# Kernel tuning notes

Hardware: AMD Instinct MI355X
Metric: run time of the kernel (lower is better)

## Reference

```python
import jax, jax.numpy as jnp
import numpy as np

DIM = 128
K = 4
B, H, W = 2, 256, 256
DEFORM_WEIGHT = 0.3


def conv2d(x, w, b, pad):
    # x [B,C,H,W], w [O,I,kh,kw], stride 1
    y = jax.lax.conv_general_dilated(
        x, w, (1, 1), [(pad, pad), (pad, pad)],
        dimension_numbers=('NCHW', 'OIHW', 'NCHW'))
    return y + b[None, :, None, None]


def gelu(x):
    return jax.nn.gelu(x, approximate=False)  # torch nn.GELU default (erf)


def grid_sample_k(feat, grid):
    """Bilinear grid_sample, padding_mode='border', align_corners=True.
    feat: [B,C,H,W]; grid: [B,K,H,W,2] (x,y) in [-1,1]. Returns [B,C,K,H,W]."""
    Bn, C, Hh, Ww = feat.shape
    px = (grid[..., 0] + 1.0) * 0.5 * (Ww - 1)
    py = (grid[..., 1] + 1.0) * 0.5 * (Hh - 1)
    px = jnp.clip(px, 0.0, Ww - 1)
    py = jnp.clip(py, 0.0, Hh - 1)
    x0 = jnp.floor(px).astype(jnp.int32)
    y0 = jnp.floor(py).astype(jnp.int32)
    x1 = jnp.minimum(x0 + 1, Ww - 1)
    y1 = jnp.minimum(y0 + 1, Hh - 1)
    wx = (px - x0)[:, None]  # [B,1,K,H,W]
    wy = (py - y0)[:, None]
    featf = feat.reshape(Bn, C, Hh * Ww)

    def gather(yi, xi):
        idx = (yi * Ww + xi).reshape(Bn, -1)  # [B, K*H*W]
        g = jax.vmap(lambda f, i: f[:, i])(featf, idx)  # [B,C,K*H*W]
        return g.reshape(Bn, C, *yi.shape[1:])

    v00 = gather(y0, x0)
    v01 = gather(y0, x1)
    v10 = gather(y1, x0)
    v11 = gather(y1, x1)
    return (v00 * (1 - wx) * (1 - wy) + v01 * wx * (1 - wy)
            + v10 * (1 - wx) * wy + v11 * wx * wy)


def setup_inputs() -> dict:
    key = jax.random.key(0)
    ks = jax.random.split(key, 16)
    nrm = lambda k, shape, s: jax.random.normal(k, shape, dtype=jnp.float32) * s
    return {
        'query_feat': jax.random.normal(ks[0], (B, DIM, H, W), dtype=jnp.float32),
        'key_feat': jax.random.normal(ks[1], (B, DIM, H, W), dtype=jnp.float32),
        # offset_net: Conv(dim,dim,3) -> GELU -> Conv(dim,2K,3); small scale keeps offsets sane
        'ow1': nrm(ks[2], (DIM, DIM, 3, 3), 0.02), 'ob1': jnp.zeros((DIM,), jnp.float32),
        'ow2': nrm(ks[3], (2 * K, DIM, 3, 3), 0.01), 'ob2': jnp.zeros((2 * K,), jnp.float32),
        # weight_net: Conv(dim,dim//4,3) -> GELU -> Conv(dim//4,K,1)
        'ww1': nrm(ks[4], (DIM // 4, DIM, 3, 3), 0.05), 'wb1': jnp.zeros((DIM // 4,), jnp.float32),
        'ww2': nrm(ks[5], (K, DIM // 4, 1, 1), 0.05), 'wb2': jnp.zeros((K,), jnp.float32),
        # fusion_conv: Conv(dim,dim,1) -> GELU -> Conv(dim,dim,1)
        'fw1': nrm(ks[6], (DIM, DIM, 1, 1), 0.05), 'fb1': jnp.zeros((DIM,), jnp.float32),
        'fw2': nrm(ks[7], (DIM, DIM, 1, 1), 0.05), 'fb2': jnp.zeros((DIM,), jnp.float32),
    }


def reference(query_feat, key_feat, ow1, ob1, ow2, ob2, ww1, wb1, ww2, wb2,
              fw1, fb1, fw2, fb2):
    offsets = conv2d(gelu(conv2d(query_feat, ow1, ob1, 1)), ow2, ob2, 1)  # [B,2K,H,W]
    wlog = conv2d(gelu(conv2d(query_feat, ww1, wb1, 1)), ww2, wb2, 0)     # [B,K,H,W]
    Bn, C, Hh, Ww = key_feat.shape
    Kp = wlog.shape[1]
    off = offsets.reshape(Bn, Kp, 2, Hh, Ww).transpose(0, 1, 3, 4, 2)  # [B,K,H,W,2]
    gy, gx = jnp.meshgrid(jnp.linspace(-1.0, 1.0, Hh),
                          jnp.linspace(-1.0, 1.0, Ww), indexing='ij')
    base = jnp.stack([gx, gy], axis=-1).astype(off.dtype)  # [H,W,2] (x,y)
    scale = jnp.array([Ww / 2.0, Hh / 2.0], dtype=off.dtype)
    grid = jnp.clip(base + off / scale, -1.0, 1.0)  # [B,K,H,W,2]
    sampled = grid_sample_k(key_feat, grid)  # [B,C,K,H,W]
    wsoft = jax.nn.softmax(wlog, axis=1)[:, None]  # [B,1,K,H,W]
    agg = (sampled * wsoft).sum(axis=2)  # [B,C,H,W]
    fused = conv2d(gelu(conv2d(agg, fw1, fb1, 0)), fw2, fb2, 0)
    return query_feat + fused * DEFORM_WEIGHT
```

## Files before the change

kernel.cpp:

```cpp
#include <hip/hip_runtime.h>
#include <hip/hip_fp16.h>

typedef unsigned short u16;
typedef __attribute__((ext_vector_type(8))) short bf16x8;
typedef __attribute__((ext_vector_type(4))) float f32x4;

constexpr int B_ = 2, C_ = 128, H_ = 256, W_ = 256, P_ = H_ * W_;
constexpr int HP_ = 258, WP_ = 258;

union HU { __half2 h; unsigned int u; };

__device__ __forceinline__ float bf2f(u16 u) {
  union { unsigned int i; float f; } v; v.i = ((unsigned int)u) << 16; return v.f;
}
__device__ __forceinline__ u16 f2bf(float f) {
  union { float f; unsigned int i; } v; v.f = f;
  return (u16)((v.i + 0x7fffu + ((v.i >> 16) & 1u)) >> 16);
}
__device__ __forceinline__ float gelu_f(float x) {
  float u = x * (1.5957691216057308f + 0.071354816272f * x * x);
  return x / (1.0f + __expf(-u));
}

__device__ __forceinline__ void async16(const u16* g, u16* l) {
  __builtin_amdgcn_global_load_lds(
      (const __attribute__((address_space(1))) unsigned int*)g,
      (__attribute__((address_space(3))) unsigned int*)l, 16, 0, 0);
}

__global__ __launch_bounds__(256) void prologue(
    const float* __restrict__ q, const float* __restrict__ key,
    const float* __restrict__ ow1, const float* __restrict__ ow2,
    const float* __restrict__ ww1, const float* __restrict__ fw1,
    const float* __restrict__ fw2,
    u16* __restrict__ qpad, u16* __restrict__ keyn, u16* __restrict__ t1pad,
    u16* __restrict__ wb) {
  __shared__ u16 l[64 * 66];
  const int id = blockIdx.x, tid = threadIdx.x;
  if (id < 8192) {
    int z = id >> 10, r = id & 1023;
    int bx = r & 3, by = r >> 2;
    const float* in; u16* out; int OW, opad;
    if (z < 4) { in = q; out = qpad; OW = WP_; opad = 1; }
    else { z -= 4; in = key; out = keyn; OW = W_; opad = 0; }
    int b = z >> 1, c0 = (z & 1) * 64;
    int h = by, w0 = bx * 64;
    for (int it = 0; it < 4; ++it) {
      int lin = it * 256 + tid;
      int c = lin >> 4, w4 = (lin & 15) * 4;
      float4 v = *(const float4*)&in[(((size_t)b * C_ + c0 + c) * H_ + h) * W_ + w0 + w4];
      l[c * 66 + w4 + 0] = f2bf(v.x);
      l[c * 66 + w4 + 1] = f2bf(v.y);
      l[c * 66 + w4 + 2] = f2bf(v.z);
      l[c * 66 + w4 + 3] = f2bf(v.w);
    }
    __syncthreads();
    int OH = (opad ? HP_ : H_);
    for (int it = 0; it < 8; ++it) {
      int lin = it * 256 + tid;
      int w = lin >> 5, c = (lin & 31) * 2;
      unsigned val = (unsigned)l[c * 66 + w] | ((unsigned)l[(c + 1) * 66 + w] << 16);
      *(unsigned*)&out[(((size_t)b * OH + h + opad) * OW + (w0 + w + opad)) * C_ + c0 + c] = val;
    }
  } else if (id < 10256) {
    int j = id - 8192;
    u16* buf = (j < 1032) ? qpad : t1pad;
    int idx = ((j < 1032) ? j : j - 1032) * 256 + tid;
    int c = idx & 127;
    int t = idx >> 7;
    int pos = t % 258;
    int side = (t / 258) & 3;
    int b = t / (258 * 4);
    int h, w;
    if (side == 0) { h = 0; w = pos; }
    else if (side == 1) { h = 257; w = pos; }
    else if (side == 2) { h = pos; w = 0; }
    else { h = pos; w = 257; }
    buf[(((size_t)b * HP_ + h) * WP_ + w) * C_ + c] = 0;
  } else {
    int idx = (id - 10256) * 256 + tid;
    float v;
    if (idx < 184320) {
      int e = idx & 7, lr = (idx >> 3) & 15, kb = (idx >> 7) & 3;
      int t = idx >> 9;
      int g = t % 10, u = t / 10;
      int cq = u & 3, tap = u >> 2;
      int ci = cq * 32 + kb * 8 + e, co = g * 16 + lr;
      v = (co < 128) ? ow1[(co * 128 + ci) * 9 + tap]
                     : ww1[((co - 128) * 128 + ci) * 9 + tap];
    } else if (idx < 202752) {
      int j = idx - 184320;
      int e = j & 7, lr = (j >> 3) & 15, kb = (j >> 7) & 3;
      int cq = (j >> 9) & 3, tap = j >> 11;
      int ci = cq * 32 + kb * 8 + e, co = lr;
      v = (co < 8) ? ow2[(co * 128 + ci) * 9 + tap] : 0.0f;
    } else if (idx < 219136) {
      v = fw1[idx - 202752];
    } else {
      v = fw2[idx - 219136];
    }
    wb[idx] = f2bf(v);
  }
}

__global__ __launch_bounds__(512, 4) void conv3_big(
    const u16* __restrict__ A, const u16* __restrict__ Wf,
    const float* __restrict__ bias1, const float* __restrict__ bias2,
    u16* __restrict__ outb, u16* __restrict__ outw) {
  constexpr int RPX = 36, ROWU = RPX * 32;
  __shared__ __align__(16) u16 As[6 * ROWU];
  const int tid = threadIdx.x, lane = tid & 63, wave = tid >> 6;
  const int id = blockIdx.x;
  const int s = id >> 3;
  const int h0 = (((id & 7) << 3) | (s & 7)) << 2;
  const int w0 = ((s >> 3) & 7) << 5;
  const int b = s >> 6;
  const int wr = wave >> 1, wc = wave & 1;
  const int wn = wc * 80;
  const int lr = lane & 15, kq = lane >> 4;
  const int gbase = wn >> 4;

  int preA[2][3];
#pragma unroll
  for (int i = 0; i < 2; i++)
#pragma unroll
    for (int kx = 0; kx < 3; kx++) {
      int pxv = i * 16 + lr + kx;
      preA[i][kx] = (pxv * 4 + (kq ^ ((pxv >> 1) & 3))) * 8;
    }

  f32x4 acc[2][5];
#pragma unroll
  for (int i = 0; i < 2; i++)
#pragma unroll
    for (int j = 0; j < 5; j++) { f32x4 z = {0.f, 0.f, 0.f, 0.f}; acc[i][j] = z; }

  for (int cq = 0; cq < 4; ++cq) {
    const int ci0 = cq * 32;
    __syncthreads();
    for (int i = tid; i < 864; i += 512) {
      int ry = i / 144;
      int rem = i - ry * 144;
      int px = rem >> 2, c8 = rem & 3;
      int g = c8 ^ ((px >> 1) & 3);
      async16(A + ((size_t)(b * HP_ + h0 + ry) * WP_ + (w0 + px)) * 128 + ci0 + g * 8,
              As + i * 8);
    }
    __syncthreads();
#pragma unroll
    for (int tap = 0; tap < 9; ++tap) {
      const int ky = tap / 3, kx = tap % 3;
      bf16x8 bfr[5], af[2];
#pragma unroll
      for (int j = 0; j < 5; ++j)
        bfr[j] = *(const bf16x8*)&Wf[(size_t)((((tap * 4 + cq) * 10 + gbase + j) * 4 + kq) * 16 + lr) * 8];
#pragma unroll
      for (int i = 0; i < 2; ++i)
        af[i] = *(const bf16x8*)&As[(wr + ky) * ROWU + preA[i][kx]];
#pragma unroll
      for (int i = 0; i < 2; i++)
#pragma unroll
        for (int j = 0; j < 5; j++)
          acc[i][j] = __builtin_amdgcn_mfma_f32_16x16x32_bf16(af[i], bfr[j], acc[i][j], 0, 0, 0);
    }
  }

  const int h = h0 + wr;
#pragma unroll
  for (int i = 0; i < 2; i++) {
#pragma unroll
    for (int j = 0; j < 5; j++) {
      const int co = wn + j * 16 + lr;
#pragma unroll
      for (int r = 0; r < 4; r++) {
        const int w = w0 + i * 16 + kq * 4 + r;
        float v = acc[i][j][r];
        if (co < 128) {
          v = gelu_f(v + bias1[co]);
          outb[(((size_t)b * HP_ + h + 1) * WP_ + (w + 1)) * 128 + co] = f2bf(v);
        } else {
          v = gelu_f(v + bias2[co - 128]);
          outw[((size_t)b * P_ + (size_t)h * W_ + w) * 32 + (co - 128)] = f2bf(v);
        }
      }
    }
  }
}

__global__ __launch_bounds__(256) void conv_off(
    const u16* __restrict__ A, const u16* __restrict__ Wf,
    const float* __restrict__ bias,
    const u16* __restrict__ w1b, const float* __restrict__ ww2,
    const float* __restrict__ wb2, uint4* __restrict__ desc) {
  constexpr int RPX = 66, ROWU = RPX * 32;
  __shared__ __align__(16) u16 As[2][6 * ROWU];
  float* off_lds = (float*)As;
  const int tid = threadIdx.x, lane = tid & 63, wave = tid >> 6;
  const int id = blockIdx.x;
  const int s = id >> 3;
  const int h0 = (((id & 7) << 3) | (s & 7)) << 2;
  const int w0 = ((s >> 3) & 3) << 6;
  const int b = s >> 5;
  const int lr = lane & 15, kq = lane >> 4;

  int preA[4][3];
#pragma unroll
  for (int i = 0; i < 4; i++)
#pragma unroll
    for (int kx = 0; kx < 3; kx++) {
      int pxv = i * 16 + lr + kx;
      preA[i][kx] = (pxv * 4 + (kq ^ ((pxv >> 1) & 3))) * 8;
    }

  f32x4 acc[4];
#pragma unroll
  for (int i = 0; i < 4; i++) { f32x4 z = {0.f, 0.f, 0.f, 0.f}; acc[i] = z; }

  for (int r = 0; r < 2; ++r) {
    __syncthreads();
#pragma unroll
    for (int half = 0; half < 2; ++half) {
      const int ci0 = (r * 2 + half) * 32;
      for (int i = tid; i < 1584; i += 256) {
        int ry = i / 264;
        int rem = i - ry * 264;
        int px = rem >> 2, c8 = rem & 3;
        int g = c8 ^ ((px >> 1) & 3);
        async16(A + ((size_t)(b * HP_ + h0 + ry) * WP_ + (w0 + px)) * 128 + ci0 + g * 8,
                As[half] + i * 8);
      }
    }
    __syncthreads();
#pragma unroll
    for (int half = 0; half < 2; ++half) {
      const int cq = r * 2 + half;
      const u16* Ac = As[half];
#pragma unroll
      for (int tap = 0; tap < 9; ++tap) {
        const int ky = tap / 3, kx = tap % 3;
        bf16x8 bw = *(const bf16x8*)&Wf[(size_t)(((tap * 4 + cq) * 4 + kq) * 16 + lr) * 8];
        bf16x8 af[4];
#pragma unroll
        for (int i = 0; i < 4; ++i)
          af[i] = *(const bf16x8*)&Ac[(wave + ky) * ROWU + preA[i][kx]];
#pragma unroll
        for (int i = 0; i < 4; i++)
          acc[i] = __builtin_amdgcn_mfma_f32_16x16x32_bf16(af[i], bw, acc[i], 0, 0, 0);
      }
    }
  }

  __syncthreads();
#pragma unroll
  for (int i = 0; i < 4; i++) {
#pragma unroll
    for (int r = 0; r < 4; r++) {
      if (lr < 8) {
        int px = i * 16 + (lane >> 4) * 4 + r;
        off_lds[(wave * 64 + px) * 9 + lr] = acc[i][r] + bias[lr];
      }
    }
  }
  __syncthreads();

  const int pp = tid;
  const int h = h0 + (pp >> 6), w = w0 + (pp & 63);
  const int pix = b * P_ + h * W_ + w;
  const u16* wp = w1b + (size_t)pix * 32;
  float f[32];
#pragma unroll
  for (int i = 0; i < 32; i += 2) {
    unsigned u = *(const unsigned*)&wp[i];
    f[i] = bf2f((u16)u); f[i + 1] = bf2f((u16)(u >> 16));
  }
  float lg[4];
#pragma unroll
  for (int k = 0; k < 4; k++) {
    float sacc = wb2[k];
#pragma unroll
    for (int i = 0; i < 32; i++) sacc = fmaf(ww2[k * 32 + i], f[i], sacc);
    lg[k] = sacc;
  }
  float mx = fmaxf(fmaxf(lg[0], lg[1]), fmaxf(lg[2], lg[3]));
  float e[4], sum = 0.f;
#pragma unroll
  for (int k = 0; k < 4; k++) { e[k] = __expf(lg[k] - mx); sum += e[k]; }
  const float inv = 1.0f / sum;
#pragma unroll
  for (int k = 0; k < 4; k++) {
    float ox = off_lds[pp * 9 + 2 * k], oy = off_lds[pp * 9 + 2 * k + 1];
    float gx = (2.0f * w / 255.0f - 1.0f) + ox * (1.0f / 128.0f);
    float gy = (2.0f * h / 255.0f - 1.0f) + oy * (1.0f / 128.0f);
    gx = fminf(fmaxf(gx, -1.f), 1.f);
    gy = fminf(fmaxf(gy, -1.f), 1.f);
    float px = fminf(fmaxf((gx + 1.f) * 127.5f, 0.f), 255.f);
    float py = fminf(fmaxf((gy + 1.f) * 127.5f, 0.f), 255.f);
    int x0 = (int)px, y0 = (int)py;
    int x1 = min(x0 + 1, 255), y1 = min(y0 + 1, 255);
    float wx = px - x0, wy = py - y0;
    float wk = e[k] * inv;
    float w00 = (1.f - wx) * (1.f - wy) * wk, w01 = wx * (1.f - wy) * wk;
    float w10 = (1.f - wx) * wy * wk,         w11 = wx * wy * wk;
    HU t01, t23;
    t01.h = __floats2half2_rn(w00, w01);
    t23.h = __floats2half2_rn(w10, w11);
    uint4 d;
    d.x = (unsigned)(y0 * 256 + x0) | ((unsigned)(x1 - x0) << 16) | ((unsigned)(y1 - y0) << 17);
    d.y = t01.u; d.z = t23.u; d.w = 0;
    desc[(size_t)pix * 4 + k] = d;
  }
}

__global__ __launch_bounds__(512, 4) void sample_fuse(
    const uint4* __restrict__ desc, const u16* __restrict__ keyn,
    const u16* __restrict__ W1, const u16* __restrict__ W2,
    const float* __restrict__ b1, const float* __restrict__ b2,
    const float* __restrict__ resid, float* __restrict__ out) {
  __shared__ __align__(16) u16 SM[128 * 128];
  __shared__ __align__(16) u16 T2[128 * 136];
  const int tid = threadIdx.x, lane = tid & 63, wave = tid >> 6;
  const int h = blockIdx.y, w0 = blockIdx.x * 128;
  const int b = blockIdx.z;
  const int wr = wave >> 1, wc = wave & 1;
  const int wm = wr * 32, wn = wc * 64;
  const int lr = lane & 15, kq = lane >> 4;
  const int sw = lr & 7;

  {
    const u16* kb = keyn + (size_t)b * (P_ * C_) + 2 * lane;
    const int pxbase = wave * 16;
    const int pixs = __builtin_amdgcn_readfirstlane(b * P_ + h * W_ + w0 + pxbase);
    const int half64 = (lane >> 5) * 64;
    const int gg = (lane >> 2) & 7;
    const int e2 = (lane & 3) * 2;
    for (int p = 0; p < 16; p += 2) {
      uint4 dA[4], dB[4];
#pragma unroll
      for (int k = 0; k < 4; ++k) dA[k] = desc[(size_t)(pixs + p) * 4 + k];
#pragma unroll
      for (int k = 0; k < 4; ++k) dB[k] = desc[(size_t)(pixs + p + 1) * 4 + k];
      unsigned vA[4][4], vB[4][4];
#pragma unroll
      for (int k = 0; k < 4; ++k) {
        const u16* c0 = kb + ((int)(dA[k].x & 0xFFFFu) << 7);
        const int o01 = (int)((dA[k].x >> 16) & 1u) << 7;
        const int o10 = (int)((dA[k].x >> 17) & 1u) << 15;
        vA[k][0] = *(const unsigned*)(c0);
        vA[k][1] = *(const unsigned*)(c0 + o01);
        vA[k][2] = *(const unsigned*)(c0 + o10);
        vA[k][3] = *(const unsigned*)(c0 + o10 + o01);
      }
#pragma unroll
      for (int k = 0; k < 4; ++k) {
        const u16* c0 = kb + ((int)(dB[k].x & 0xFFFFu) << 7);
        const int o01 = (int)((dB[k].x >> 16) & 1u) << 7;
        const int o10 = (int)((dB[k].x >> 17) & 1u) << 15;
        vB[k][0] = *(const unsigned*)(c0);
        vB[k][1] = *(const unsigned*)(c0 + o01);
        vB[k][2] = *(const unsigned*)(c0 + o10);
        vB[k][3] = *(const unsigned*)(c0 + o10 + o01);
      }
      float p0A[4], p1A[4], p0B[4], p1B[4];
#pragma unroll
      for (int k = 0; k < 4; ++k) {
        HU t01, t23; t01.u = dA[k].y; t23.u = dA[k].z;
        float2 wA = __half22float2(t01.h);
        float2 wB = __half22float2(t23.h);
        float s0 = wA.x * bf2f((u16)vA[k][0]);
        s0 = fmaf(wA.y, bf2f((u16)vA[k][1]), s0);
        s0 = fmaf(wB.x, bf2f((u16)vA[k][2]), s0);
        s0 = fmaf(wB.y, bf2f((u16)vA[k][3]), s0);
        p0A[k] = s0;
        float s1 = wA.x * bf2f((u16)(vA[k][0] >> 16));
        s1 = fmaf(wA.y, bf2f((u16)(vA[k][1] >> 16)), s1);
        s1 = fmaf(wB.x, bf2f((u16)(vA[k][2] >> 16)), s1);
        s1 = fmaf(wB.y, bf2f((u16)(vA[k][3] >> 16)), s1);
        p1A[k] = s1;
      }
#pragma unroll
      for (int k = 0; k < 4; ++k) {
        HU t01, t23; t01.u = dB[k].y; t23.u = dB[k].z;
        float2 wA = __half22float2(t01.h);
        float2 wB = __half22float2(t23.h);
        float s0 = wA.x * bf2f((u16)vB[k][0]);
        s0 = fmaf(wA.y, bf2f((u16)vB[k][1]), s0);
        s0 = fmaf(wB.x, bf2f((u16)vB[k][2]), s0);
        s0 = fmaf(wB.y, bf2f((u16)vB[k][3]), s0);
        p0B[k] = s0;
        float s1 = wA.x * bf2f((u16)(vB[k][0] >> 16));
        s1 = fmaf(wA.y, bf2f((u16)(vB[k][1] >> 16)), s1);
        s1 = fmaf(wB.x, bf2f((u16)(vB[k][2] >> 16)), s1);
        s1 = fmaf(wB.y, bf2f((u16)(vB[k][3] >> 16)), s1);
        p1B[k] = s1;
      }
      float a0A = (p0A[0] + p0A[1]) + (p0A[2] + p0A[3]);
      float a1A = (p1A[0] + p1A[1]) + (p1A[2] + p1A[3]);
      float a0B = (p0B[0] + p0B[1]) + (p0B[2] + p0B[3]);
      float a1B = (p1B[0] + p1B[1]) + (p1B[2] + p1B[3]);
      const int pxA = pxbase + p, pxB = pxbase + p + 1;
      unsigned uA = ((unsigned)f2bf(a1A) << 16) | (unsigned)f2bf(a0A);
      unsigned uB = ((unsigned)f2bf(a1B) << 16) | (unsigned)f2bf(a0B);
      *(unsigned*)&SM[pxA * 128 + half64 + ((gg ^ (pxA & 7)) << 3) + e2] = uA;
      *(unsigned*)&SM[pxB * 128 + half64 + ((gg ^ (pxB & 7)) << 3) + e2] = uB;
    }
  }

  f32x4 acc[2][4];
#pragma unroll
  for (int i = 0; i < 2; i++)
#pragma unroll
    for (int j = 0; j < 4; j++) { f32x4 z = {0.f, 0.f, 0.f, 0.f}; acc[i][j] = z; }

  for (int c = 0; c < 2; ++c) {
    const int ci0 = c << 6;
    const u16* Wb = W1 + ci0;
    __syncthreads();
    for (int i = tid; i < 1024; i += 512) {
      int r = i >> 3, cb = i & 7;
      async16(Wb + r * 128 + ((cb ^ (r & 7)) << 3), T2 + i * 8);
    }
    __syncthreads();
#pragma unroll
    for (int ks = 0; ks < 2; ++ks) {
      const int kb = ks * 4 + kq;
      bf16x8 af[2], bfr[4];
#pragma unroll
      for (int i = 0; i < 2; i++)
        af[i] = *(const bf16x8*)&SM[(wm + i * 16 + lr) * 128 + ci0 + ((kb ^ sw) << 3)];
#pragma unroll
      for (int j = 0; j < 4; j++)
        bfr[j] = *(const bf16x8*)&T2[(wn + j * 16 + lr) * 64 + ((kb ^ sw) << 3)];
#pragma unroll
      for (int i = 0; i < 2; i++)
#pragma unroll
        for (int j = 0; j < 4; j++)
          acc[i][j] = __builtin_amdgcn_mfma_f32_16x16x32_bf16(af[i], bfr[j], acc[i][j], 0, 0, 0);
    }
  }
  __syncthreads();

  for (int i = tid; i < 2048; i += 512) {
    int r = i >> 4, sl = i & 15;
    int g = sl ^ (r & 7);
    async16(W2 + r * 128 + g * 8, SM + i * 8);
  }
#pragma unroll
  for (int i = 0; i < 2; i++)
#pragma unroll
    for (int j = 0; j < 4; j++) {
      const int co = wn + j * 16 + lr;
#pragma unroll
      for (int r = 0; r < 4; r++) {
        const int px = wm + i * 16 + kq * 4 + r;
        T2[px * 136 + co] = f2bf(gelu_f(acc[i][j][r] + b1[co]));
      }
    }
  __syncthreads();

#pragma unroll
  for (int i = 0; i < 2; i++)
#pragma unroll
    for (int j = 0; j < 4; j++) { f32x4 z = {0.f, 0.f, 0.f, 0.f}; acc[i][j] = z; }
#pragma unroll
  for (int ks = 0; ks < 4; ++ks) {
    const int kc = ks * 4 + kq;
    bf16x8 af[2], bfr[4];
#pragma unroll
    for (int i = 0; i < 2; i++)
      af[i] = *(const bf16x8*)&T2[(wm + i * 16 + lr) * 136 + kc * 8];
#pragma unroll
    for (int j = 0; j < 4; j++) {
      int rr = wn + j * 16 + lr;
      bfr[j] = *(const bf16x8*)&SM[rr * 128 + (kc ^ (rr & 7)) * 8];
    }
#pragma unroll
    for (int i = 0; i < 2; i++)
#pragma unroll
      for (int j = 0; j < 4; j++)
        acc[i][j] = __builtin_amdgcn_mfma_f32_16x16x32_bf16(af[i], bfr[j], acc[i][j], 0, 0, 0);
  }

#pragma unroll
  for (int i = 0; i < 2; i++) {
#pragma unroll
    for (int j = 0; j < 4; j++) {
      const int co = wn + j * 16 + lr;
      const int w = w0 + wm + i * 16 + kq * 4;
      size_t idx = ((size_t)b * 128 + co) * (size_t)P_ + (size_t)h * W_ + w;
      float4 rv = *(const float4*)&resid[idx];
      float bi = b2[co];
      float4 ov;
      ov.x = rv.x + 0.3f * (acc[i][j][0] + bi);
      ov.y = rv.y + 0.3f * (acc[i][j][1] + bi);
      ov.z = rv.z + 0.3f * (acc[i][j][2] + bi);
      ov.w = rv.w + 0.3f * (acc[i][j][3] + bi);
      *(float4*)&out[idx] = ov;
    }
  }
}

extern "C" void kernel_launch(void* const* d_in, const int* in_sizes, int n_in,
                              void* d_out, int out_size, void* d_ws, size_t ws_size,
                              hipStream_t stream) {
  (void)in_sizes; (void)n_in; (void)out_size; (void)ws_size;
  const float* q   = (const float*)d_in[0];
  const float* key = (const float*)d_in[1];
  const float* ow1 = (const float*)d_in[2];
  const float* ob1 = (const float*)d_in[3];
  const float* ow2 = (const float*)d_in[4];
  const float* ob2 = (const float*)d_in[5];
  const float* ww1 = (const float*)d_in[6];
  const float* wb1 = (const float*)d_in[7];
  const float* ww2 = (const float*)d_in[8];
  const float* wb2 = (const float*)d_in[9];
  const float* fw1 = (const float*)d_in[10];
  const float* fb1 = (const float*)d_in[11];
  const float* fw2 = (const float*)d_in[12];
  const float* fb2 = (const float*)d_in[13];
  float* out = (float*)d_out;
  char* ws = (char*)d_ws;

  u16* qpad  = (u16*)(ws);
  u16* t1pad = (u16*)(ws + 34080768);
  u16* keyn  = (u16*)(ws + 68161536);
  u16* w1b   = (u16*)(ws + 101715968);
  u16* wbuf  = (u16*)(ws + 110104576);
  uint4* desc = (uint4*)ws;

  prologue<<<11176, 256, 0, stream>>>(q, key, ow1, ow2, ww1, fw1, fw2,
                                      qpad, keyn, t1pad, wbuf);
  conv3_big<<<1024, 512, 0, stream>>>(qpad, wbuf, ob1, wb1, t1pad, w1b);
  conv_off<<<512, 256, 0, stream>>>(t1pad, wbuf + 184320, ob2, w1b, ww2, wb2, desc);
  sample_fuse<<<dim3(2, 256, 2), 512, 0, stream>>>(desc, keyn, wbuf + 202752,
                                                   wbuf + 219136, fb1, fb2, q, out);
}
```

Baseline: 345.0 us.

## Double-buffer activations and weights in LDS with async prefetch in conv3_big

Result: no change. 340.8 us (-1.2%).

```diff
diff --git a/kernel.cpp b/kernel.cpp
--- a/kernel.cpp
+++ b/kernel.cpp
@@ -108,7 +108,9 @@
     const float* __restrict__ bias1, const float* __restrict__ bias2,
     u16* __restrict__ outb, u16* __restrict__ outw) {
   constexpr int RPX = 36, ROWU = RPX * 32;
-  __shared__ __align__(16) u16 As[6 * ROWU];
+  constexpr int WTILE = 5120;
+  __shared__ __align__(16) u16 As[2][6 * ROWU];
+  __shared__ __align__(16) u16 Wl[2][WTILE];
   const int tid = threadIdx.x, lane = tid & 63, wave = tid >> 6;
   const int id = blockIdx.x;
   const int s = id >> 3;
@@ -129,39 +131,79 @@
       preA[i][kx] = (pxv * 4 + (kq ^ ((pxv >> 1) & 3))) * 8;
     }
 
+  size_t soff0, soff1;
+  int doff0, doff1;
+  const bool has2 = (tid + 512 < 864);
+  {
+    int i = tid;
+    int ry = i / 144;
+    int rem = i - ry * 144;
+    int px = rem >> 2, c8 = rem & 3;
+    int g = c8 ^ ((px >> 1) & 3);
+    soff0 = ((size_t)(b * HP_ + h0 + ry) * WP_ + (w0 + px)) * 128 + g * 8;
+    doff0 = i * 8;
+  }
+  {
+    int i = (tid + 512 < 864) ? tid + 512 : tid;
+    int ry = i / 144;
+    int rem = i - ry * 144;
+    int px = rem >> 2, c8 = rem & 3;
+    int g = c8 ^ ((px >> 1) & 3);
+    soff1 = ((size_t)(b * HP_ + h0 + ry) * WP_ + (w0 + px)) * 128 + g * 8;
+    doff1 = i * 8;
+  }
+  const bool whas2 = (tid < 128);
+  const int wt0 = tid * 8, wt1 = (tid + 512) * 8;
+
   f32x4 acc[2][5];
 #pragma unroll
   for (int i = 0; i < 2; i++)
 #pragma unroll
     for (int j = 0; j < 5; j++) { f32x4 z = {0.f, 0.f, 0.f, 0.f}; acc[i][j] = z; }
 
+  async16(A + soff0, As[0] + doff0);
+  if (has2) async16(A + soff1, As[0] + doff1);
+  async16(Wf + wt0, Wl[0] + wt0);
+  if (whas2) async16(Wf + wt1, Wl[0] + wt1);
+  __syncthreads();
+
   for (int cq = 0; cq < 4; ++cq) {
-    const int ci0 = cq * 32;
-    __syncthreads();
-    for (int i = tid; i < 864; i += 512) {
-      int ry = i / 144;
-      int rem = i - ry * 144;
-      int px = rem >> 2, c8 = rem & 3;
-      int g = c8 ^ ((px >> 1) & 3);
-      async16(A + ((size_t)(b * HP_ + h0 + ry) * WP_ + (w0 + px)) * 128 + ci0 + g * 8,
-              As + i * 8);
-    }
-    __syncthreads();
 #pragma unroll
     for (int tap = 0; tap < 9; ++tap) {
       const int ky = tap / 3, kx = tap % 3;
+      const int par = (cq + tap) & 1;
+      if (tap < 8) {
+        const u16* wsrc = Wf + (size_t)((tap + 1) * 4 + cq) * WTILE;
+        u16* wdst = Wl[par ^ 1];
+        async16(wsrc + wt0, wdst + wt0);
+        if (whas2) async16(wsrc + wt1, wdst + wt1);
+      } else if (cq < 3) {
+        const u16* wsrc = Wf + (size_t)(cq + 1) * WTILE;
+        u16* wdst = Wl[par ^ 1];
+        async16(wsrc + wt0, wdst + wt0);
+        if (whas2) async16(wsrc + wt1, wdst + wt1);
+      }
+      if (tap == 0 && cq < 3) {
+        const int ci0 = (cq + 1) * 32;
+        u16* dst = As[(cq + 1) & 1];
+        async16(A + soff0 + ci0, dst + doff0);
+        if (has2) async16(A + soff1 + ci0, dst + doff1);
+      }
+      const u16* Ac = As[cq & 1];
+      const u16* Wc = Wl[par];
       bf16x8 bfr[5], af[2];
 #pragma unroll
       for (int j = 0; j < 5; ++j)
-        bfr[j] = *(const bf16x8*)&Wf[(size_t)((((tap * 4 + cq) * 10 + gbase + j) * 4 + kq) * 16 + lr) * 8];
+        bfr[j] = *(const bf16x8*)&Wc[(gbase + j) * 512 + lane * 8];
 #pragma unroll
       for (int i = 0; i < 2; ++i)
-        af[i] = *(const bf16x8*)&As[(wr + ky) * ROWU + preA[i][kx]];
+        af[i] = *(const bf16x8*)&Ac[(wr + ky) * ROWU + preA[i][kx]];
 #pragma unroll
       for (int i = 0; i < 2; i++)
 #pragma unroll
         for (int j = 0; j < 5; j++)
           acc[i][j] = __builtin_amdgcn_mfma_f32_16x16x32_bf16(af[i], bfr[j], acc[i][j], 0, 0, 0);
+      if (!(cq == 3 && tap == 8)) __syncthreads();
     }
   }
 
```
